# Kernel tuning notes

Hardware: AMD Instinct MI355X
Metric: run time of the kernel (lower is better)

## Reference

```python
import jax, jax.numpy as jnp
import numpy as np

NEG_INF = -1e30


def setup_inputs() -> dict:
    B, S, H, N, T = 128, 512, 512, 256, 40960
    key = jax.random.key(0)
    ks = jax.random.split(key, 20)
    sc = 1.0 / np.sqrt(H)
    inp = {
        'tok_feat': jax.random.normal(ks[0], (B, S, H), jnp.float32),
        'ast_h': jax.random.normal(ks[1], (T, H), jnp.float32),
        'cfg_feat': jax.random.normal(ks[2], (B, N, H), jnp.float32),
        'W_tok': jax.random.normal(ks[3], (H, H), jnp.float32) * sc,
        'b_tok': jax.random.normal(ks[4], (H,), jnp.float32) * 0.01,
        'v_tok': jax.random.normal(ks[5], (H,), jnp.float32) * sc,
        'c_tok': jnp.float32(0.0),
        'W_ast': jax.random.normal(ks[6], (H, H), jnp.float32) * sc,
        'b_ast': jax.random.normal(ks[7], (H,), jnp.float32) * 0.01,
        'v_ast': jax.random.normal(ks[8], (H,), jnp.float32) * sc,
        'c_ast': jnp.float32(0.0),
        'W_cfg': jax.random.normal(ks[9], (H, H), jnp.float32) * sc,
        'b_cfg': jax.random.normal(ks[10], (H,), jnp.float32) * 0.01,
        'v_cfg': jax.random.normal(ks[11], (H,), jnp.float32) * sc,
        'c_cfg': jnp.float32(0.0),
        'W_fuse': jax.random.normal(ks[12], (3 * H, H), jnp.float32) * (1.0 / np.sqrt(3 * H)),
        'b_fuse': jax.random.normal(ks[13], (H,), jnp.float32) * 0.01,
        'tok_len': jax.random.randint(ks[14], (B,), 1, S + 1, jnp.int64),
        # ragged AST: sorted segment ids covering T nodes, here equal-size segments
        'node_seg': jnp.repeat(jnp.arange(B, dtype=jnp.int32), T // B),
        'cfg_node_mask': jax.random.randint(ks[15], (B, N), 0, 2, jnp.int32).at[:, 0].set(1),
    }
    return inp


def reference(tok_feat, ast_h, cfg_feat,
              W_tok, b_tok, v_tok, c_tok,
              W_ast, b_ast, v_ast, c_ast,
              W_cfg, b_cfg, v_cfg, c_cfg,
              W_fuse, b_fuse,
              tok_len, node_seg, cfg_node_mask):
    B, S, H = tok_feat.shape
    N = cfg_feat.shape[1]

    # ---- Token modality: masked softmax attention pooling ----
    tok_logit = jnp.tanh(tok_feat @ W_tok + b_tok) @ v_tok + c_tok          # [B,S]
    tok_mask = jnp.arange(S)[None, :] < tok_len[:, None]                    # [B,S]
    tok_w = jax.nn.softmax(jnp.where(tok_mask, tok_logit, NEG_INF), axis=1)
    tok_pool = jnp.einsum('bs,bsh->bh', tok_w, tok_feat)                    # [B,H]

    # ---- AST modality: ragged segment softmax attention pooling ----
    ast_logit = jnp.tanh(ast_h @ W_ast + b_ast) @ v_ast + c_ast             # [T]
    seg_max = jax.ops.segment_max(ast_logit, node_seg, num_segments=B)
    e = jnp.exp(ast_logit - seg_max[node_seg])
    denom = jax.ops.segment_sum(e, node_seg, num_segments=B)
    ast_w = e / denom[node_seg]                                             # [T]
    ast_pool = jax.ops.segment_sum(ast_w[:, None] * ast_h, node_seg, num_segments=B)  # [B,H]

    # ---- CFG modality: masked sigmoid-gated pooling ----
    cfg_logit = jnp.tanh(cfg_feat @ W_cfg + b_cfg) @ v_cfg + c_cfg          # [B,N]
    gate = jax.nn.sigmoid(cfg_logit) * cfg_node_mask.astype(cfg_feat.dtype)
    cfg_pool = jnp.einsum('bn,bnh->bh', gate, cfg_feat)                     # [B,H]

    # ---- Modal fusion ----
    concat = jnp.concatenate([tok_pool, ast_pool, cfg_pool], axis=1)        # [B,3H]
    code_feat = jnp.tanh(concat @ W_fuse + b_fuse)                          # [B,H]
    return code_feat
```

## Files before the change

kernel.cpp:

```cpp
#include <hip/hip_runtime.h>
#include <stdint.h>

#define HD 512

typedef __bf16 bf16x8 __attribute__((ext_vector_type(8)));
typedef __bf16 bf16x4 __attribute__((ext_vector_type(4)));
typedef float  f32x4  __attribute__((ext_vector_type(4)));

union BF8U { uint4 u; bf16x8 v; };

__device__ __forceinline__ float fast_tanh(float x) {
  x = fminf(15.f, fmaxf(-15.f, x));
  float e = __expf(2.f * x);
  return (e - 1.f) * __builtin_amdgcn_rcpf(e + 1.f);
}
__device__ __forceinline__ float fast_sigmoid(float x) {
  return __builtin_amdgcn_rcpf(1.f + __expf(-x));
}

__global__ void zero_kernel(float4* __restrict__ p, int n) {
  int i = blockIdx.x * 256 + threadIdx.x;
  if (i < n) p[i] = make_float4(0.f, 0.f, 0.f, 0.f);
}

__global__ void prep_w_kernel(const float* __restrict__ W0, const float* __restrict__ W1,
                              const float* __restrict__ W2, unsigned short* __restrict__ WbAll) {
  int mat = blockIdx.x >> 6;
  int chunk = blockIdx.x & 63;
  const float* W = (mat == 0) ? W0 : ((mat == 1) ? W1 : W2);
  int np = chunk >> 4, kt = chunk & 15;
  int t = threadIdx.x;
  int jl = t & 127, kh = t >> 7;
  int j = np * 128 + jl;
  int nt = jl >> 4;
  unsigned short* base = WbAll + (size_t)mat * 262144 + (size_t)chunk * 4096 + nt * 512;
#pragma unroll
  for (int i = 0; i < 16; ++i) {
    int kk = kh * 16 + i;
    float v = W[(size_t)(kt * 32 + kk) * HD + j];
    int l = (kk >> 3) * 16 + (jl & 15);
    int jj = kk & 7;
    union { __bf16 h; unsigned short u; } cv;
    cv.h = (__bf16)v;
    base[l * 8 + jj] = cv.u;
  }
}

__global__ __launch_bounds__(512, 2) void gemm_logit_kernel(
    const float* __restrict__ A, const unsigned short* __restrict__ Wb,
    const float* __restrict__ bias, const float* __restrict__ vvec,
    const int* __restrict__ rowLim,
    float* __restrict__ logit)
{
  int bm = blockIdx.x;
  size_t m0 = (size_t)bm * 64;

  if (rowLim) {
    bool i64 = (rowLim[1] == 0);
    int b = (int)(m0 >> 9);
    int len = i64 ? rowLim[2 * b] : rowLim[b];
    if ((int)(m0 & 511) >= len) return;
  }

  int tid = threadIdx.x, wave = tid >> 6, lane = tid & 63;
  int wn = wave;

  __shared__ __align__(16) char AshB[2][4096];
  __shared__ float redS[8][64];

  const float* aSrc = A + (m0 + (tid >> 3)) * HD + (tid & 7) * 4;
  const int rowS = tid >> 3, qS = tid & 7;
  const int srW = rowS >> 1;
  const int wA = srW * 128 + 16 * ((((rowS & 1) << 2) + (qS >> 1)) ^ (srW & 7)) + (qS & 1) * 8;

  const char* srcB = (const char*)Wb + (size_t)(wn >> 1) * 131072 +
                     (wn & 1) * 4096 + lane * 16;

  const int aRd = ((lane & 15) >> 1) * 128 +
                  16 * ((4 * (lane & 1) + (lane >> 4)) ^ ((lane & 15) >> 1));

  float4 a4;
  auto loadA = [&](float4& dst, int kt) {
    dst = *(const float4*)(aSrc + kt * 32);
  };
  auto writeA = [&](int buf, const float4& ar) {
    bf16x4 w0;
    w0[0] = (__bf16)ar.x; w0[1] = (__bf16)ar.y; w0[2] = (__bf16)ar.z; w0[3] = (__bf16)ar.w;
    *(bf16x4*)(&AshB[buf][0] + wA) = w0;
  };
  auto loadB = [&](bf16x8 (&dst)[4], int kt) {
    const char* sB = srcB + (size_t)kt * 8192;
#pragma unroll
    for (int ntl = 0; ntl < 4; ++ntl) {
      BF8U bu;
      bu.u = *(const uint4*)(sB + ntl * 1024);
      dst[ntl] = bu.v;
    }
  };

  f32x4 acc[4][4];
#pragma unroll
  for (int i = 0; i < 4; ++i)
#pragma unroll
    for (int j = 0; j < 4; ++j) acc[i][j] = (f32x4){0.f, 0.f, 0.f, 0.f};

  {
    float4 t4;
    loadA(t4, 0);
    writeA(0, t4);
    loadA(a4, 1);
    asm volatile("s_waitcnt lgkmcnt(0)" ::: "memory");
    __builtin_amdgcn_s_barrier();
  }

  bf16x8 bf[4];
#pragma unroll 2
  for (int kt = 0; kt < 16; ++kt) {
    loadB(bf, kt);
    const char* aBuf = &AshB[kt & 1][0];
    bf16x8 af[4];
#pragma unroll
    for (int mt = 0; mt < 4; ++mt)
      af[mt] = *(const bf16x8*)(aBuf + mt * 1024 + aRd);
#pragma unroll
    for (int mt = 0; mt < 4; ++mt)
#pragma unroll
      for (int ntl = 0; ntl < 4; ++ntl)
        acc[mt][ntl] = __builtin_amdgcn_mfma_f32_16x16x32_bf16(af[mt], bf[ntl], acc[mt][ntl], 0, 0, 0);
    if (kt < 15) {
      writeA((kt + 1) & 1, a4);
      if (kt < 14) loadA(a4, kt + 2);
      asm volatile("s_waitcnt lgkmcnt(0)" ::: "memory");
      __builtin_amdgcn_s_barrier();
    }
  }

  float part[4][4];
#pragma unroll
  for (int mt = 0; mt < 4; ++mt)
#pragma unroll
    for (int i = 0; i < 4; ++i) part[mt][i] = 0.f;

  const int colBase = wn * 64;
#pragma unroll
  for (int ntl = 0; ntl < 4; ++ntl) {
    int j = colBase + ntl * 16 + (lane & 15);
    float bj = bias[j], vj = vvec[j];
#pragma unroll
    for (int mt = 0; mt < 4; ++mt)
#pragma unroll
      for (int i = 0; i < 4; ++i)
        part[mt][i] += fast_tanh(acc[mt][ntl][i] + bj) * vj;
  }
#pragma unroll
  for (int off = 8; off >= 1; off >>= 1)
#pragma unroll
    for (int mt = 0; mt < 4; ++mt)
#pragma unroll
      for (int i = 0; i < 4; ++i)
        part[mt][i] += __shfl_xor(part[mt][i], off, 64);

  if ((lane & 15) == 0) {
    int rloc = (lane >> 4) * 4;
#pragma unroll
    for (int mt = 0; mt < 4; ++mt)
#pragma unroll
      for (int i = 0; i < 4; ++i)
        redS[wn][mt * 16 + rloc + i] = part[mt][i];
  }
  __syncthreads();
  if (tid < 64) {
    float s = 0.f;
#pragma unroll
    for (int w = 0; w < 8; ++w) s += redS[w][tid];
    logit[m0 + tid] = s;
  }
}

__global__ void seg_bounds_kernel(const int* __restrict__ seg, int* __restrict__ ss,
                                  int* __restrict__ se, int T) {
  int t = blockIdx.x * 256 + threadIdx.x;
  if (t >= T) return;
  int s = seg[t];
  if (t == 0 || seg[t - 1] != s) ss[s] = t;
  if (t == T - 1 || seg[t + 1] != s) se[s] = t + 1;
}

__global__ void pool_tok_kernel(const float* __restrict__ feat, const float* __restrict__ logit,
                                const int* __restrict__ tl, float* __restrict__ pool) {
  int b = blockIdx.x, ch = blockIdx.y;
  int tid = threadIdx.x;
  bool i64 = (tl[1] == 0);
  int len = i64 ? tl[2 * b] : tl[b];
  if (ch * 128 >= len) return;
  const float* lg = logit + b * 512;
  float x0 = (tid < len) ? lg[tid] : -1e30f;
  float x1 = (tid + 256 < len) ? lg[tid + 256] : -1e30f;
  float m = fmaxf(x0, x1);
#pragma unroll
  for (int off = 32; off; off >>= 1) m = fmaxf(m, __shfl_xor(m, off, 64));
  __shared__ float redm[4], reds[4];
  int wv = tid >> 6, ln = tid & 63;
  if (ln == 0) redm[wv] = m;
  __syncthreads();
  float bm = fmaxf(fmaxf(redm[0], redm[1]), fmaxf(redm[2], redm[3]));
  float s = ((tid < len) ? __expf(x0 - bm) : 0.f) + ((tid + 256 < len) ? __expf(x1 - bm) : 0.f);
#pragma unroll
  for (int off = 32; off; off >>= 1) s += __shfl_xor(s, off, 64);
  if (ln == 0) reds[wv] = s;
  __syncthreads();
  float bs = reds[0] + reds[1] + reds[2] + reds[3];
  float rb = __builtin_amdgcn_rcpf(bs);
  __shared__ float wsh[128];
  if (tid < 128) {
    int sidx = ch * 128 + tid;
    wsh[tid] = (sidx < len) ? __expf(lg[sidx] - bm) * rb : 0.f;
  }
  __syncthreads();
  int cnt = min(128, len - ch * 128);
  int h = tid * 2;
  float2 acc = make_float2(0.f, 0.f);
  const float* fb = feat + ((size_t)b * 512 + ch * 128) * HD + h;
#pragma unroll 4
  for (int s2 = 0; s2 < cnt; ++s2) {
    float2 f = *(const float2*)(fb + (size_t)s2 * HD);
    acc.x += wsh[s2] * f.x; acc.y += wsh[s2] * f.y;
  }
  atomicAdd(&pool[b * 512 + h], acc.x);
  atomicAdd(&pool[b * 512 + h + 1], acc.y);
}

__global__ void pool_ast_kernel(const float* __restrict__ ast, const float* __restrict__ logit,
                                const int* __restrict__ ss, const int* __restrict__ se,
                                float* __restrict__ pool) {
  int b = blockIdx.x, ch = blockIdx.y;
  int tid = threadIdx.x;
  int t0 = ss[b], t1 = se[b];
  int len = t1 - t0;
  if (len <= 0) return;
  float m = -1e30f;
  for (int t = t0 + tid; t < t1; t += 256) m = fmaxf(m, logit[t]);
#pragma unroll
  for (int off = 32; off; off >>= 1) m = fmaxf(m, __shfl_xor(m, off, 64));
  __shared__ float redm[4], reds[4];
  int wv = tid >> 6, ln = tid & 63;
  if (ln == 0) redm[wv] = m;
  __syncthreads();
  float bm = fmaxf(fmaxf(redm[0], redm[1]), fmaxf(redm[2], redm[3]));
  float s = 0.f;
  for (int t = t0 + tid; t < t1; t += 256) s += __expf(logit[t] - bm);
#pragma unroll
  for (int off = 32; off; off >>= 1) s += __shfl_xor(s, off, 64);
  if (ln == 0) reds[wv] = s;
  __syncthreads();
  float bs = reds[0] + reds[1] + reds[2] + reds[3];
  float r = __builtin_amdgcn_rcpf(bs);
  int per = (len + 3) >> 2;
  int a0 = t0 + ch * per;
  int a1 = min(t1, a0 + per);
  __shared__ float wsh[128];
  int h = tid * 2;
  float2 acc = make_float2(0.f, 0.f);
  for (int base = a0; base < a1; base += 128) {
    int cnt = min(128, a1 - base);
    __syncthreads();
    if (tid < cnt) wsh[tid] = __expf(logit[base + tid] - bm) * r;
    __syncthreads();
    for (int s2 = 0; s2 < cnt; ++s2) {
      float2 f = *(const float2*)(ast + (size_t)(base + s2) * HD + h);
      acc.x += wsh[s2] * f.x; acc.y += wsh[s2] * f.y;
    }
  }
  atomicAdd(&pool[b * 512 + h], acc.x);
  atomicAdd(&pool[b * 512 + h + 1], acc.y);
}

__global__ void pool_cfg_kernel(const float* __restrict__ feat, const float* __restrict__ logit,
                                const int* __restrict__ mask, const float* __restrict__ cptr,
                                float* __restrict__ pool) {
  int b = blockIdx.x, ch = blockIdx.y;
  int tid = threadIdx.x;
  float cc = cptr[0];
  __shared__ float gsh[128];
  int n0 = ch * 128;
  if (tid < 128) {
    int n = n0 + tid;
    float g = fast_sigmoid(logit[b * 256 + n] + cc);
    gsh[tid] = mask[b * 256 + n] ? g : 0.f;
  }
  __syncthreads();
  int h = tid * 2;
  float2 acc = make_float2(0.f, 0.f);
  const float* fb = feat + ((size_t)b * 256 + n0) * HD + h;
#pragma unroll 4
  for (int s = 0; s < 128; ++s) {
    float2 f = *(const float2*)(fb + (size_t)s * HD);
    acc.x += gsh[s] * f.x; acc.y += gsh[s] * f.y;
  }
  atomicAdd(&pool[b * 512 + h], acc.x);
  atomicAdd(&pool[b * 512 + h + 1], acc.y);
}

__global__ void fuse_partial_kernel(const float* __restrict__ pools,
                                    const float* __restrict__ Wf,
                                    float* __restrict__ fpart) {
  int bg = blockIdx.x, kc = blockIdx.y;
  int tid = threadIdx.x;
  int bq = tid >> 7, jt = tid & 127;
  __shared__ float psh[8][128];
  for (int idx = tid; idx < 8 * 128; idx += 256) {
    int bb = idx >> 7, kk = idx & 127;
    int i = kc * 128 + kk;
    psh[bb][kk] = pools[(size_t)(i >> 9) * 65536 + (size_t)(bg * 8 + bb) * 512 + (i & 511)];
  }
  __syncthreads();
  f32x4 acc[4];
#pragma unroll
  for (int bb = 0; bb < 4; ++bb) acc[bb] = (f32x4){0.f, 0.f, 0.f, 0.f};
  const float* wrow = Wf + (size_t)(kc * 128) * 512 + jt * 4;
#pragma unroll 4
  for (int k = 0; k < 128; ++k) {
    float4 wv = *(const float4*)(wrow + (size_t)k * 512);
#pragma unroll
    for (int bb = 0; bb < 4; ++bb) {
      float p = psh[bq * 4 + bb][k];
      acc[bb][0] += p * wv.x; acc[bb][1] += p * wv.y;
      acc[bb][2] += p * wv.z; acc[bb][3] += p * wv.w;
    }
  }
  float* dst = fpart + (size_t)kc * 65536 + (size_t)(bg * 8 + bq * 4) * 512 + jt * 4;
#pragma unroll
  for (int bb = 0; bb < 4; ++bb)
    *(f32x4*)(dst + (size_t)bb * 512) = acc[bb];
}

__global__ void finalize_kernel(const float* __restrict__ fpart, const float* __restrict__ bfuse,
                                float* __restrict__ out) {
  int idx = blockIdx.x * 256 + threadIdx.x;
  float s = bfuse[idx & 511];
#pragma unroll
  for (int kc = 0; kc < 12; ++kc) s += fpart[(size_t)kc * 65536 + idx];
  out[idx] = fast_tanh(s);
}

static constexpr size_t OFF_WB_TOK = 0;
static constexpr size_t OFF_WB_AST = 512 * 1024;
static constexpr size_t OFF_WB_CFG = 1024 * 1024;
static constexpr size_t OFF_LG_TOK = 1536 * 1024;
static constexpr size_t OFF_LG_AST = OFF_LG_TOK + 65536 * 4;
static constexpr size_t OFF_LG_CFG = OFF_LG_AST + 40960 * 4;
static constexpr size_t OFF_POOLS  = OFF_LG_CFG + 32768 * 4;
static constexpr size_t OFF_SS     = OFF_POOLS + 3 * 65536 * 4;
static constexpr size_t OFF_SE     = OFF_SS + 512;
static constexpr size_t ZERO_BYTES = 3 * 65536 * 4 + 1024;
static constexpr size_t OFF_FPART  = OFF_SE + 512;

extern "C" void kernel_launch(void* const* d_in, const int* in_sizes, int n_in,
                              void* d_out, int out_size, void* d_ws, size_t ws_size,
                              hipStream_t stream) {
  const float* tok_feat = (const float*)d_in[0];
  const float* ast_h    = (const float*)d_in[1];
  const float* cfg_feat = (const float*)d_in[2];
  const float* W_tok = (const float*)d_in[3];
  const float* b_tok = (const float*)d_in[4];
  const float* v_tok = (const float*)d_in[5];
  const float* W_ast = (const float*)d_in[7];
  const float* b_ast = (const float*)d_in[8];
  const float* v_ast = (const float*)d_in[9];
  const float* W_cfg = (const float*)d_in[11];
  const float* b_cfg = (const float*)d_in[12];
  const float* v_cfg = (const float*)d_in[13];
  const float* c_cfg = (const float*)d_in[14];
  const float* W_fuse = (const float*)d_in[15];
  const float* b_fuse = (const float*)d_in[16];
  const int* tok_len  = (const int*)d_in[17];
  const int* node_seg = (const int*)d_in[18];
  const int* cfg_mask = (const int*)d_in[19];

  const int M_tok = in_sizes[0] / HD;
  const int T_ast = in_sizes[1] / HD;
  const int M_cfg = in_sizes[2] / HD;

  char* ws = (char*)d_ws;
  unsigned short* wbAll = (unsigned short*)(ws + OFF_WB_TOK);
  unsigned short* wbTok = (unsigned short*)(ws + OFF_WB_TOK);
  unsigned short* wbAst = (unsigned short*)(ws + OFF_WB_AST);
  unsigned short* wbCfg = (unsigned short*)(ws + OFF_WB_CFG);
  float* lgTok = (float*)(ws + OFF_LG_TOK);
  float* lgAst = (float*)(ws + OFF_LG_AST);
  float* lgCfg = (float*)(ws + OFF_LG_CFG);
  float* pools = (float*)(ws + OFF_POOLS);
  int*   ss    = (int*)(ws + OFF_SS);
  int*   se    = (int*)(ws + OFF_SE);
  float* fpart = (float*)(ws + OFF_FPART);

  {
    int n4 = (int)(ZERO_BYTES / 16);
    zero_kernel<<<(n4 + 255) / 256, 256, 0, stream>>>((float4*)(ws + OFF_POOLS), n4);
  }

  prep_w_kernel<<<192, 256, 0, stream>>>(W_tok, W_ast, W_cfg, wbAll);
  seg_bounds_kernel<<<(T_ast + 255) / 256, 256, 0, stream>>>(node_seg, ss, se, T_ast);

  gemm_logit_kernel<<<M_tok / 64, 512, 0, stream>>>(tok_feat, wbTok, b_tok, v_tok, tok_len, lgTok);
  pool_tok_kernel<<<dim3(128, 4), 256, 0, stream>>>(tok_feat, lgTok, tok_len, pools + 0 * 65536);

  gemm_logit_kernel<<<T_ast / 64, 512, 0, stream>>>(ast_h, wbAst, b_ast, v_ast, nullptr, lgAst);
  pool_ast_kernel<<<dim3(128, 4), 256, 0, stream>>>(ast_h, lgAst, ss, se, pools + 1 * 65536);

  gemm_logit_kernel<<<M_cfg / 64, 512, 0, stream>>>(cfg_feat, wbCfg, b_cfg, v_cfg, nullptr, lgCfg);
  pool_cfg_kernel<<<dim3(128, 2), 256, 0, stream>>>(cfg_feat, lgCfg, cfg_mask, c_cfg, pools + 2 * 65536);

  fuse_partial_kernel<<<dim3(16, 12), 256, 0, stream>>>(pools, W_fuse, fpart);
  finalize_kernel<<<256, 256, 0, stream>>>(fpart, b_fuse, (float*)d_out);
}
```

Measured before the change: 190.7 us.

## Merge per-modality GEMM and pooling launches into combined grid kernels

Folds the zeroing, weight-prep and segment-bounds kernels into one setup launch. It also merges the three per-modality logit GEMMs into one grid and the three pooling kernels into another, dispatching on block index. This removes launch gaps and serialization between modalities, so blocks from different modalities can run together and fill the GPU. In exchange, ss/se are no longer zeroed, so an empty AST segment would read uninitialized bounds.

Result: faster. 160.1 us (-16.0%).

```diff
diff --git a/kernel.cpp b/kernel.cpp
--- a/kernel.cpp
+++ b/kernel.cpp
@@ -18,49 +18,67 @@
   return __builtin_amdgcn_rcpf(1.f + __expf(-x));
 }
 
-__global__ void zero_kernel(float4* __restrict__ p, int n) {
-  int i = blockIdx.x * 256 + threadIdx.x;
-  if (i < n) p[i] = make_float4(0.f, 0.f, 0.f, 0.f);
-}
-
-__global__ void prep_w_kernel(const float* __restrict__ W0, const float* __restrict__ W1,
-                              const float* __restrict__ W2, unsigned short* __restrict__ WbAll) {
-  int mat = blockIdx.x >> 6;
-  int chunk = blockIdx.x & 63;
-  const float* W = (mat == 0) ? W0 : ((mat == 1) ? W1 : W2);
-  int np = chunk >> 4, kt = chunk & 15;
-  int t = threadIdx.x;
-  int jl = t & 127, kh = t >> 7;
-  int j = np * 128 + jl;
-  int nt = jl >> 4;
-  unsigned short* base = WbAll + (size_t)mat * 262144 + (size_t)chunk * 4096 + nt * 512;
-#pragma unroll
-  for (int i = 0; i < 16; ++i) {
-    int kk = kh * 16 + i;
-    float v = W[(size_t)(kt * 32 + kk) * HD + j];
-    int l = (kk >> 3) * 16 + (jl & 15);
-    int jj = kk & 7;
-    union { __bf16 h; unsigned short u; } cv;
-    cv.h = (__bf16)v;
-    base[l * 8 + jj] = cv.u;
-  }
-}
-
-__global__ __launch_bounds__(512, 2) void gemm_logit_kernel(
-    const float* __restrict__ A, const unsigned short* __restrict__ Wb,
-    const float* __restrict__ bias, const float* __restrict__ vvec,
-    const int* __restrict__ rowLim,
-    float* __restrict__ logit)
+__global__ void setup_kernel(const float* __restrict__ W0, const float* __restrict__ W1,
+                             const float* __restrict__ W2, unsigned short* __restrict__ WbAll,
+                             float4* __restrict__ zdst, int nz,
+                             const int* __restrict__ seg, int* __restrict__ ss,
+                             int* __restrict__ se, int T) {
+  int blk = blockIdx.x, t = threadIdx.x;
+  if (blk < 192) {
+    int mat = blk >> 6, chunk = blk & 63;
+    const float* W = (mat == 0) ? W0 : ((mat == 1) ? W1 : W2);
+    int np = chunk >> 4, kt = chunk & 15;
+    int jl = t & 127, kh = t >> 7;
+    int j = np * 128 + jl;
+    int nt = jl >> 4;
+    unsigned short* base = WbAll + (size_t)mat * 262144 + (size_t)chunk * 4096 + nt * 512;
+#pragma unroll
+    for (int i = 0; i < 16; ++i) {
+      int kk = kh * 16 + i;
+      float v = W[(size_t)(kt * 32 + kk) * HD + j];
+      int l = (kk >> 3) * 16 + (jl & 15);
+      int jj = kk & 7;
+      union { __bf16 h; unsigned short u; } cv;
+      cv.h = (__bf16)v;
+      base[l * 8 + jj] = cv.u;
+    }
+  } else if (blk < 384) {
+    int i = (blk - 192) * 256 + t;
+    if (i < nz) zdst[i] = make_float4(0.f, 0.f, 0.f, 0.f);
+  } else {
+    int tt = (blk - 384) * 256 + t;
+    if (tt < T) {
+      int s = seg[tt];
+      if (tt == 0 || seg[tt - 1] != s) ss[s] = tt;
+      if (tt == T - 1 || seg[tt + 1] != s) se[s] = tt + 1;
+    }
+  }
+}
+
+__global__ __launch_bounds__(512, 2) void gemm_all_kernel(
+    const float* __restrict__ A0, const float* __restrict__ A1, const float* __restrict__ A2,
+    const unsigned short* __restrict__ WbAll,
+    const float* __restrict__ b0, const float* __restrict__ v0,
+    const float* __restrict__ b1, const float* __restrict__ v1,
+    const float* __restrict__ b2, const float* __restrict__ v2,
+    const int* __restrict__ tokLen, int nTok, int nAst,
+    float* __restrict__ lg0, float* __restrict__ lg1, float* __restrict__ lg2)
 {
   int bm = blockIdx.x;
-  size_t m0 = (size_t)bm * 64;
-
-  if (rowLim) {
-    bool i64 = (rowLim[1] == 0);
-    int b = (int)(m0 >> 9);
-    int len = i64 ? rowLim[2 * b] : rowLim[b];
-    if ((int)(m0 & 511) >= len) return;
-  }
+  const float* A; const unsigned short* Wb; const float* bias; const float* vvec;
+  float* logit; int lb;
+  if (bm < nTok) {
+    lb = bm; A = A0; Wb = WbAll; bias = b0; vvec = v0; logit = lg0;
+    bool i64 = (tokLen[1] == 0);
+    int b = lb >> 3;
+    int len = i64 ? tokLen[2 * b] : tokLen[b];
+    if (((lb & 7) * 64) >= len) return;
+  } else if (bm < nTok + nAst) {
+    lb = bm - nTok; A = A1; Wb = WbAll + 262144; bias = b1; vvec = v1; logit = lg1;
+  } else {
+    lb = bm - nTok - nAst; A = A2; Wb = WbAll + 524288; bias = b2; vvec = v2; logit = lg2;
+  }
+  size_t m0 = (size_t)lb * 64;
 
   int tid = threadIdx.x, wave = tid >> 6, lane = tid & 63;
   int wn = wave;
@@ -177,128 +195,114 @@
   }
 }
 
-__global__ void seg_bounds_kernel(const int* __restrict__ seg, int* __restrict__ ss,
-                                  int* __restrict__ se, int T) {
-  int t = blockIdx.x * 256 + threadIdx.x;
-  if (t >= T) return;
-  int s = seg[t];
-  if (t == 0 || seg[t - 1] != s) ss[s] = t;
-  if (t == T - 1 || seg[t + 1] != s) se[s] = t + 1;
-}
-
-__global__ void pool_tok_kernel(const float* __restrict__ feat, const float* __restrict__ logit,
-                                const int* __restrict__ tl, float* __restrict__ pool) {
-  int b = blockIdx.x, ch = blockIdx.y;
-  int tid = threadIdx.x;
-  bool i64 = (tl[1] == 0);
-  int len = i64 ? tl[2 * b] : tl[b];
-  if (ch * 128 >= len) return;
-  const float* lg = logit + b * 512;
-  float x0 = (tid < len) ? lg[tid] : -1e30f;
-  float x1 = (tid + 256 < len) ? lg[tid + 256] : -1e30f;
-  float m = fmaxf(x0, x1);
-#pragma unroll
-  for (int off = 32; off; off >>= 1) m = fmaxf(m, __shfl_xor(m, off, 64));
+__global__ void pool_all_kernel(
+    const float* __restrict__ tokf, const float* __restrict__ lgT, const int* __restrict__ tl,
+    const float* __restrict__ astf, const float* __restrict__ lgA,
+    const int* __restrict__ ss, const int* __restrict__ se,
+    const float* __restrict__ cfgf, const float* __restrict__ lgC,
+    const int* __restrict__ mask, const float* __restrict__ cptr,
+    float* __restrict__ pools)
+{
+  int b = blockIdx.x, chz = blockIdx.y, tid = threadIdx.x;
   __shared__ float redm[4], reds[4];
+  __shared__ float wsh[128];
   int wv = tid >> 6, ln = tid & 63;
-  if (ln == 0) redm[wv] = m;
-  __syncthreads();
-  float bm = fmaxf(fmaxf(redm[0], redm[1]), fmaxf(redm[2], redm[3]));
-  float s = ((tid < len) ? __expf(x0 - bm) : 0.f) + ((tid + 256 < len) ? __expf(x1 - bm) : 0.f);
-#pragma unroll
-  for (int off = 32; off; off >>= 1) s += __shfl_xor(s, off, 64);
-  if (ln == 0) reds[wv] = s;
-  __syncthreads();
-  float bs = reds[0] + reds[1] + reds[2] + reds[3];
-  float rb = __builtin_amdgcn_rcpf(bs);
-  __shared__ float wsh[128];
-  if (tid < 128) {
-    int sidx = ch * 128 + tid;
-    wsh[tid] = (sidx < len) ? __expf(lg[sidx] - bm) * rb : 0.f;
-  }
-  __syncthreads();
-  int cnt = min(128, len - ch * 128);
-  int h = tid * 2;
-  float2 acc = make_float2(0.f, 0.f);
-  const float* fb = feat + ((size_t)b * 512 + ch * 128) * HD + h;
+
+  if (chz < 4) {
+    int ch = chz;
+    bool i64 = (tl[1] == 0);
+    int len = i64 ? tl[2 * b] : tl[b];
+    if (ch * 128 >= len) return;
+    const float* lg = lgT + b * 512;
+    float x0 = (tid < len) ? lg[tid] : -1e30f;
+    float x1 = (tid + 256 < len) ? lg[tid + 256] : -1e30f;
+    float m = fmaxf(x0, x1);
+#pragma unroll
+    for (int off = 32; off; off >>= 1) m = fmaxf(m, __shfl_xor(m, off, 64));
+    if (ln == 0) redm[wv] = m;
+    __syncthreads();
+    float bm = fmaxf(fmaxf(redm[0], redm[1]), fmaxf(redm[2], redm[3]));
+    float s = ((tid < len) ? __expf(x0 - bm) : 0.f) + ((tid + 256 < len) ? __expf(x1 - bm) : 0.f);
+#pragma unroll
+    for (int off = 32; off; off >>= 1) s += __shfl_xor(s, off, 64);
+    if (ln == 0) reds[wv] = s;
+    __syncthreads();
+    float bs = reds[0] + reds[1] + reds[2] + reds[3];
+    float rb = __builtin_amdgcn_rcpf(bs);
+    if (tid < 128) {
+      int sidx = ch * 128 + tid;
+      wsh[tid] = (sidx < len) ? __expf(lg[sidx] - bm) * rb : 0.f;
+    }
+    __syncthreads();
+    int cnt = min(128, len - ch * 128);
+    int h = tid * 2;
+    float2 acc = make_float2(0.f, 0.f);
+    const float* fb = tokf + ((size_t)b * 512 + ch * 128) * HD + h;
 #pragma unroll 4
-  for (int s2 = 0; s2 < cnt; ++s2) {
-    float2 f = *(const float2*)(fb + (size_t)s2 * HD);
-    acc.x += wsh[s2] * f.x; acc.y += wsh[s2] * f.y;
-  }
-  atomicAdd(&pool[b * 512 + h], acc.x);
-  atomicAdd(&pool[b * 512 + h + 1], acc.y);
-}
-
-__global__ void pool_ast_kernel(const float* __restrict__ ast, const float* __restrict__ logit,
-                                const int* __restrict__ ss, const int* __restrict__ se,
-                                float* __restrict__ pool) {
-  int b = blockIdx.x, ch = blockIdx.y;
-  int tid = threadIdx.x;
-  int t0 = ss[b], t1 = se[b];
-  int len = t1 - t0;
-  if (len <= 0) return;
-  float m = -1e30f;
-  for (int t = t0 + tid; t < t1; t += 256) m = fmaxf(m, logit[t]);
-#pragma unroll
-  for (int off = 32; off; off >>= 1) m = fmaxf(m, __shfl_xor(m, off, 64));
-  __shared__ float redm[4], reds[4];
-  int wv = tid >> 6, ln = tid & 63;
-  if (ln == 0) redm[wv] = m;
-  __syncthreads();
-  float bm = fmaxf(fmaxf(redm[0], redm[1]), fmaxf(redm[2], redm[3]));
-  float s = 0.f;
-  for (int t = t0 + tid; t < t1; t += 256) s += __expf(logit[t] - bm);
-#pragma unroll
-  for (int off = 32; off; off >>= 1) s += __shfl_xor(s, off, 64);
-  if (ln == 0) reds[wv] = s;
-  __syncthreads();
-  float bs = reds[0] + reds[1] + reds[2] + reds[3];
-  float r = __builtin_amdgcn_rcpf(bs);
-  int per = (len + 3) >> 2;
-  int a0 = t0 + ch * per;
-  int a1 = min(t1, a0 + per);
-  __shared__ float wsh[128];
-  int h = tid * 2;
-  float2 acc = make_float2(0.f, 0.f);
-  for (int base = a0; base < a1; base += 128) {
-    int cnt = min(128, a1 - base);
-    __syncthreads();
-    if (tid < cnt) wsh[tid] = __expf(logit[base + tid] - bm) * r;
-    __syncthreads();
     for (int s2 = 0; s2 < cnt; ++s2) {
-      float2 f = *(const float2*)(ast + (size_t)(base + s2) * HD + h);
+      float2 f = *(const float2*)(fb + (size_t)s2 * HD);
       acc.x += wsh[s2] * f.x; acc.y += wsh[s2] * f.y;
     }
-  }
-  atomicAdd(&pool[b * 512 + h], acc.x);
-  atomicAdd(&pool[b * 512 + h + 1], acc.y);
-}
-
-__global__ void pool_cfg_kernel(const float* __restrict__ feat, const float* __restrict__ logit,
-                                const int* __restrict__ mask, const float* __restrict__ cptr,
-                                float* __restrict__ pool) {
-  int b = blockIdx.x, ch = blockIdx.y;
-  int tid = threadIdx.x;
-  float cc = cptr[0];
-  __shared__ float gsh[128];
-  int n0 = ch * 128;
-  if (tid < 128) {
-    int n = n0 + tid;
-    float g = fast_sigmoid(logit[b * 256 + n] + cc);
-    gsh[tid] = mask[b * 256 + n] ? g : 0.f;
-  }
-  __syncthreads();
-  int h = tid * 2;
-  float2 acc = make_float2(0.f, 0.f);
-  const float* fb = feat + ((size_t)b * 256 + n0) * HD + h;
+    atomicAdd(&pools[b * 512 + h], acc.x);
+    atomicAdd(&pools[b * 512 + h + 1], acc.y);
+  } else if (chz < 8) {
+    int ch = chz - 4;
+    int t0 = ss[b], t1 = se[b];
+    int len = t1 - t0;
+    if (len <= 0) return;
+    float m = -1e30f;
+    for (int t = t0 + tid; t < t1; t += 256) m = fmaxf(m, lgA[t]);
+#pragma unroll
+    for (int off = 32; off; off >>= 1) m = fmaxf(m, __shfl_xor(m, off, 64));
+    if (ln == 0) redm[wv] = m;
+    __syncthreads();
+    float bm = fmaxf(fmaxf(redm[0], redm[1]), fmaxf(redm[2], redm[3]));
+    float s = 0.f;
+    for (int t = t0 + tid; t < t1; t += 256) s += __expf(lgA[t] - bm);
+#pragma unroll
+    for (int off = 32; off; off >>= 1) s += __shfl_xor(s, off, 64);
+    if (ln == 0) reds[wv] = s;
+    __syncthreads();
+    float bs = reds[0] + reds[1] + reds[2] + reds[3];
+    float r = __builtin_amdgcn_rcpf(bs);
+    int per = (len + 3) >> 2;
+    int a0 = t0 + ch * per;
+    int a1 = min(t1, a0 + per);
+    int h = tid * 2;
+    float2 acc = make_float2(0.f, 0.f);
+    for (int base = a0; base < a1; base += 128) {
+      int cnt = min(128, a1 - base);
+      __syncthreads();
+      if (tid < cnt) wsh[tid] = __expf(lgA[base + tid] - bm) * r;
+      __syncthreads();
+      for (int s2 = 0; s2 < cnt; ++s2) {
+        float2 f = *(const float2*)(astf + (size_t)(base + s2) * HD + h);
+        acc.x += wsh[s2] * f.x; acc.y += wsh[s2] * f.y;
+      }
+    }
+    atomicAdd(&pools[65536 + b * 512 + h], acc.x);
+    atomicAdd(&pools[65536 + b * 512 + h + 1], acc.y);
+  } else {
+    int ch = chz - 8;
+    float cc = cptr[0];
+    int n0 = ch * 128;
+    if (tid < 128) {
+      int n = n0 + tid;
+      float g = fast_sigmoid(lgC[b * 256 + n] + cc);
+      wsh[tid] = mask[b * 256 + n] ? g : 0.f;
+    }
+    __syncthreads();
+    int h = tid * 2;
+    float2 acc = make_float2(0.f, 0.f);
+    const float* fb = cfgf + ((size_t)b * 256 + n0) * HD + h;
 #pragma unroll 4
-  for (int s = 0; s < 128; ++s) {
-    float2 f = *(const float2*)(fb + (size_t)s * HD);
-    acc.x += gsh[s] * f.x; acc.y += gsh[s] * f.y;
-  }
-  atomicAdd(&pool[b * 512 + h], acc.x);
-  atomicAdd(&pool[b * 512 + h + 1], acc.y);
+    for (int s2 = 0; s2 < 128; ++s2) {
+      float2 f = *(const float2*)(fb + (size_t)s2 * HD);
+      acc.x += wsh[s2] * f.x; acc.y += wsh[s2] * f.y;
+    }
+    atomicAdd(&pools[131072 + b * 512 + h], acc.x);
+    atomicAdd(&pools[131072 + b * 512 + h + 1], acc.y);
+  }
 }
 
 __global__ void fuse_partial_kernel(const float* __restrict__ pools,
@@ -343,17 +347,15 @@
   out[idx] = fast_tanh(s);
 }
 
-static constexpr size_t OFF_WB_TOK = 0;
-static constexpr size_t OFF_WB_AST = 512 * 1024;
-static constexpr size_t OFF_WB_CFG = 1024 * 1024;
+static constexpr size_t OFF_WB_ALL = 0;
 static constexpr size_t OFF_LG_TOK = 1536 * 1024;
 static constexpr size_t OFF_LG_AST = OFF_LG_TOK + 65536 * 4;
 static constexpr size_t OFF_LG_CFG = OFF_LG_AST + 40960 * 4;
 static constexpr size_t OFF_POOLS  = OFF_LG_CFG + 32768 * 4;
 static constexpr size_t OFF_SS     = OFF_POOLS + 3 * 65536 * 4;
 static constexpr size_t OFF_SE     = OFF_SS + 512;
-static constexpr size_t ZERO_BYTES = 3 * 65536 * 4 + 1024;
 static constexpr size_t OFF_FPART  = OFF_SE + 512;
+static constexpr int    ZERO_N4    = (3 * 65536 * 4) / 16;
 
 extern "C" void kernel_launch(void* const* d_in, const int* in_sizes, int n_in,
                               void* d_out, int out_size, void* d_ws, size_t ws_size,
@@ -380,12 +382,10 @@
   const int M_tok = in_sizes[0] / HD;
   const int T_ast = in_sizes[1] / HD;
   const int M_cfg = in_sizes[2] / HD;
+  const int nTok = M_tok / 64, nAst = T_ast / 64, nCfg = M_cfg / 64;
 
   char* ws = (char*)d_ws;
-  unsigned short* wbAll = (unsigned short*)(ws + OFF_WB_TOK);
-  unsigned short* wbTok = (unsigned short*)(ws + OFF_WB_TOK);
-  unsigned short* wbAst = (unsigned short*)(ws + OFF_WB_AST);
-  unsigned short* wbCfg = (unsigned short*)(ws + OFF_WB_CFG);
+  unsigned short* wbAll = (unsigned short*)(ws + OFF_WB_ALL);
   float* lgTok = (float*)(ws + OFF_LG_TOK);
   float* lgAst = (float*)(ws + OFF_LG_AST);
   float* lgCfg = (float*)(ws + OFF_LG_CFG);
@@ -394,22 +394,20 @@
   int*   se    = (int*)(ws + OFF_SE);
   float* fpart = (float*)(ws + OFF_FPART);
 
-  {
-    int n4 = (int)(ZERO_BYTES / 16);
-    zero_kernel<<<(n4 + 255) / 256, 256, 0, stream>>>((float4*)(ws + OFF_POOLS), n4);
-  }
-
-  prep_w_kernel<<<192, 256, 0, stream>>>(W_tok, W_ast, W_cfg, wbAll);
-  seg_bounds_kernel<<<(T_ast + 255) / 256, 256, 0, stream>>>(node_seg, ss, se, T_ast);
-
-  gemm_logit_kernel<<<M_tok / 64, 512, 0, stream>>>(tok_feat, wbTok, b_tok, v_tok, tok_len, lgTok);
-  pool_tok_kernel<<<dim3(128, 4), 256, 0, stream>>>(tok_feat, lgTok, tok_len, pools + 0 * 65536);
-
-  gemm_logit_kernel<<<T_ast / 64, 512, 0, stream>>>(ast_h, wbAst, b_ast, v_ast, nullptr, lgAst);
-  pool_ast_kernel<<<dim3(128, 4), 256, 0, stream>>>(ast_h, lgAst, ss, se, pools + 1 * 65536);
-
-  gemm_logit_kernel<<<M_cfg / 64, 512, 0, stream>>>(cfg_feat, wbCfg, b_cfg, v_cfg, nullptr, lgCfg);
-  pool_cfg_kernel<<<dim3(128, 2), 256, 0, stream>>>(cfg_feat, lgCfg, cfg_mask, c_cfg, pools + 2 * 65536);
+  int segBlks = (T_ast + 255) / 256;
+  setup_kernel<<<384 + segBlks, 256, 0, stream>>>(
+      W_tok, W_ast, W_cfg, wbAll, (float4*)(ws + OFF_POOLS), ZERO_N4,
+      node_seg, ss, se, T_ast);
+
+  gemm_all_kernel<<<nTok + nAst + nCfg, 512, 0, stream>>>(
+      tok_feat, ast_h, cfg_feat, wbAll,
+      b_tok, v_tok, b_ast, v_ast, b_cfg, v_cfg,
+      tok_len, nTok, nAst, lgTok, lgAst, lgCfg);
+
+  pool_all_kernel<<<dim3(128, 10), 256, 0, stream>>>(
+      tok_feat, lgTok, tok_len,
+      ast_h, lgAst, ss, se,
+      cfg_feat, lgCfg, cfg_mask, c_cfg, pools);
 
   fuse_partial_kernel<<<dim3(16, 12), 256, 0, stream>>>(pools, W_fuse, fpart);
   finalize_kernel<<<256, 256, 0, stream>>>(fpart, b_fuse, (float*)d_out);
```
